# Optimization experiments

Measured on AMD Instinct MI355X. Metric: run time of the kernel, lower is better.

The kernel has to match this reference:

```python
import jax, jax.numpy as jnp
import numpy as np

HOPS = 3  # max_hops; C has HOPS+1 tables

def setup_inputs() -> dict:
    key = jax.random.key(0)
    k1, k2, k3 = jax.random.split(key, 3)
    B, M, S, V, D = 32, 512, 10, 32000, 128
    story = jax.random.randint(k1, (B, M, S), 0, V)
    hidden = jax.random.normal(k2, (B, 1, D), dtype=jnp.float32)
    # hop+1 embedding tables, initialized N(0, 0.1) like the torch module
    C = 0.1 * jax.random.normal(k3, (HOPS + 1, V, D), dtype=jnp.float32)
    return {"story": story, "hidden": hidden, "C": C}

def reference(story, hidden, C):
    # story: [B, M, S] int tokens; hidden: [B, 1, D]; C: [HOPS+1, V, D]
    u = jnp.squeeze(hidden, axis=1)  # [B, D]
    prob_logit = None
    for h in range(HOPS):
        # embedding gather + bag-sum over sentence dim -> [B, M, D]
        embed_A = jnp.take(C[h], story, axis=0).sum(axis=2)
        # dot-product attention logits against current query u
        prob_logit = jnp.einsum('bmd,bd->bm', embed_A, u)  # [B, M]
        prob = jax.nn.softmax(prob_logit, axis=1)
        # second table gather + bag-sum, then softmax-weighted combine
        embed_C = jnp.take(C[h + 1], story, axis=0).sum(axis=2)  # [B, M, D]
        o_k = jnp.einsum('bm,bmd->bd', prob, embed_C)  # [B, D]
        u = u + o_k
    return prob_logit, u
```

## Files before the change

### kernel.cpp

```cpp
#include <hip/hip_runtime.h>

#define BB 32
#define MM 512
#define SS 10
#define VV 32000
#define DD 128
#define HOPS 3
#define BM (BB * MM)
#define NCHUNK 32
#define CHM (MM / NCHUNK)
#define PSTRIDE 132
#define PAIR_UNITS ((size_t)VV * 32)

__device__ __forceinline__ unsigned bfrn(float f) {
    unsigned u = __float_as_uint(f);
    return (u + 0x7FFFu + ((u >> 16) & 1u)) >> 16;
}
__device__ __forceinline__ unsigned pk(float a, float b) { return bfrn(a) | (bfrn(b) << 16); }
__device__ __forceinline__ float bflo(unsigned q) { return __uint_as_float(q << 16); }
__device__ __forceinline__ float bfhi(unsigned q) { return __uint_as_float(q & 0xFFFF0000u); }

__device__ __forceinline__ void cvt_pair_unit(const float* __restrict__ CA,
                                              const float* __restrict__ CB,
                                              unsigned* __restrict__ dst, size_t g) {
    const size_t v = g >> 5, j = g & 31;
    const float4 a = ((const float4*)CA)[v * 32 + j];
    const float4 b = ((const float4*)CB)[v * 32 + j];
    uint4 o;
    o.x = pk(a.x, a.y);
    o.y = pk(b.x, b.y);
    o.z = pk(a.z, a.w);
    o.w = pk(b.z, b.w);
    ((uint4*)dst)[v * 32 + j] = o;
}


__global__ __launch_bounds__(256) void cvt01(const float* __restrict__ Cmat,
                                             unsigned* __restrict__ Cb01) {
    const size_t g = (size_t)blockIdx.x * 256 + threadIdx.x;
    if (g < PAIR_UNITS)
        cvt_pair_unit(Cmat, Cmat + (size_t)VV * DD, Cb01, g);
}

__device__ __forceinline__ void stage_u(const int b, const int c, const int tid,
                                        const float* __restrict__ uprev,
                                        const float* __restrict__ pin,
                                        float* __restrict__ uwrite,
                                        float* __restrict__ su) {
    if (tid < DD) {
        float v = uprev[b * DD + tid];
        if (pin) {
            float num = 0.f, dsum = 0.f;
            for (int cc = 0; cc < NCHUNK; ++cc) {
                const float* p = pin + ((size_t)b * NCHUNK + cc) * PSTRIDE;
                num += p[tid];
                dsum += p[DD];
            }
            v += num / dsum;
            if (c == 0 && uwrite) uwrite[b * DD + tid] = v;
        }
        su[tid] = v;
    }
    __syncthreads();
}

__device__ __forceinline__ void write_partial(const int b, const int c,
                                              const int w, const int lane,
                                              float nx, float ny, float den,
                                              float* __restrict__ pout,
                                              float (*sx)[64], float (*sy)[64],
                                              float* sd) {
    sx[w][lane] = nx; sy[w][lane] = ny;
    if (lane == 0) sd[w] = den;
    __syncthreads();
    if (w == 0) {
        const float ox = sx[0][lane] + sx[1][lane] + sx[2][lane] + sx[3][lane];
        const float oy = sy[0][lane] + sy[1][lane] + sy[2][lane] + sy[3][lane];
        float* prow = pout + ((size_t)b * NCHUNK + c) * PSTRIDE;
        ((float2*)prow)[lane] = make_float2(ox, oy);
        if (lane == 0) prow[DD] = sd[0] + sd[1] + sd[2] + sd[3];
    }
}

__global__ __launch_bounds__(256) void hop0_k(const int* __restrict__ story,
                                              const unsigned* __restrict__ Cb01,
                                              float* __restrict__ E1,
                                              const float* __restrict__ hidden,
                                              float* __restrict__ pout,
                                              const float* __restrict__ Cmat,
                                              unsigned* __restrict__ Cb23) {
    const int b = blockIdx.y, c = blockIdx.x;
    const int tid = threadIdx.x;
    const int w = tid >> 6, lane = tid & 63;
    __shared__ float su[DD];
    __shared__ float sx[4][64], sy[4][64];
    __shared__ float sd[4];

    stage_u(b, c, tid, hidden, nullptr, nullptr, su);
    const float2 uv = ((const float2*)su)[lane];
    const uint2* G = (const uint2*)Cb01;

    float nx = 0.f, ny = 0.f, den = 0.f;
#pragma unroll
    for (int k = 0; k < CHM / 4; ++k) {
        const int m = c * CHM + k * 4 + w;
        const int bm = b * MM + m;
        int tok[SS];
        const int* st = story + (size_t)bm * SS;
#pragma unroll
        for (int s = 0; s < SS; ++s) tok[s] = st[s];

        float ex = 0.f, ey = 0.f, rx = 0.f, ry = 0.f;
#pragma unroll
        for (int s = 0; s < SS; ++s) {
            const uint2 q = G[(size_t)tok[s] * 64 + lane];
            ex += bflo(q.x); ey += bfhi(q.x);
            rx += bflo(q.y); ry += bfhi(q.y);
        }
        float l = ex * uv.x + ey * uv.y;
#pragma unroll
        for (int off = 32; off; off >>= 1) l += __shfl_xor(l, off, 64);
        const float e = expf(l);

        ((float2*)(E1 + (size_t)bm * DD))[lane] = make_float2(rx, ry);
        nx += e * rx; ny += e * ry; den += e;
    }
    write_partial(b, c, w, lane, nx, ny, den, pout, sx, sy, sd);

    const size_t t0 = (((size_t)blockIdx.y * gridDim.x + blockIdx.x) * 256 + tid) * 4;
#pragma unroll
    for (int i = 0; i < 4; ++i) {
        const size_t g = t0 + i;
        if (g < PAIR_UNITS)
            cvt_pair_unit(Cmat + (size_t)2 * VV * DD, Cmat + (size_t)3 * VV * DD,
                          Cb23, g);
    }
}

__global__ __launch_bounds__(256) void hop1_k(const int* __restrict__ story,
                                              const unsigned* __restrict__ Cb23,
                                              const float* __restrict__ E1,
                                              float* __restrict__ E2,
                                              float* __restrict__ E3,
                                              const float* __restrict__ hidden,
                                              const float* __restrict__ pin,
                                              float* __restrict__ u1,
                                              float* __restrict__ pout) {
    const int b = blockIdx.y, c = blockIdx.x;
    const int tid = threadIdx.x;
    const int w = tid >> 6, lane = tid & 63;
    __shared__ float su[DD];
    __shared__ float sx[4][64], sy[4][64];
    __shared__ float sd[4];

    stage_u(b, c, tid, hidden, pin, u1, su);
    const float2 uv = ((const float2*)su)[lane];
    const uint2* G = (const uint2*)Cb23;

    float nx = 0.f, ny = 0.f, den = 0.f;
#pragma unroll
    for (int k = 0; k < CHM / 4; ++k) {
        const int m = c * CHM + k * 4 + w;
        const int bm = b * MM + m;
        int tok[SS];
        const int* st = story + (size_t)bm * SS;
#pragma unroll
        for (int s = 0; s < SS; ++s) tok[s] = st[s];

        const float2 ev = ((const float2*)(E1 + (size_t)bm * DD))[lane];
        float l = ev.x * uv.x + ev.y * uv.y;
#pragma unroll
        for (int off = 32; off; off >>= 1) l += __shfl_xor(l, off, 64);
        const float e = expf(l);

        float r2x = 0.f, r2y = 0.f, r3x = 0.f, r3y = 0.f;
#pragma unroll
        for (int s = 0; s < SS; ++s) {
            const uint2 q = G[(size_t)tok[s] * 64 + lane];
            r2x += bflo(q.x); r2y += bfhi(q.x);
            r3x += bflo(q.y); r3y += bfhi(q.y);
        }
        ((float2*)(E2 + (size_t)bm * DD))[lane] = make_float2(r2x, r2y);
        ((float2*)(E3 + (size_t)bm * DD))[lane] = make_float2(r3x, r3y);
        nx += e * r2x; ny += e * r2y; den += e;
    }
    write_partial(b, c, w, lane, nx, ny, den, pout, sx, sy, sd);
}

__global__ __launch_bounds__(256) void hop2_k(const float* __restrict__ E2,
                                              const float* __restrict__ E3,
                                              const float* __restrict__ u1,
                                              const float* __restrict__ pin,
                                              float* __restrict__ u2,
                                              float* __restrict__ logit,
                                              float* __restrict__ pout) {
    const int b = blockIdx.y, c = blockIdx.x;
    const int tid = threadIdx.x;
    const int w = tid >> 6, lane = tid & 63;
    __shared__ float su[DD];
    __shared__ float sx[4][64], sy[4][64];
    __shared__ float sd[4];

    stage_u(b, c, tid, u1, pin, u2, su);
    const float2 uv = ((const float2*)su)[lane];

    float nx = 0.f, ny = 0.f, den = 0.f;
#pragma unroll
    for (int k = 0; k < CHM / 4; ++k) {
        const int m = c * CHM + k * 4 + w;
        const int bm = b * MM + m;

        const float2 ev = ((const float2*)(E2 + (size_t)bm * DD))[lane];
        float l = ev.x * uv.x + ev.y * uv.y;
#pragma unroll
        for (int off = 32; off; off >>= 1) l += __shfl_xor(l, off, 64);
        if (lane == 0) logit[bm] = l;
        const float e = expf(l);

        const float2 rv = ((const float2*)(E3 + (size_t)bm * DD))[lane];
        nx += e * rv.x; ny += e * rv.y; den += e;
    }
    write_partial(b, c, w, lane, nx, ny, den, pout, sx, sy, sd);
}

__global__ __launch_bounds__(128) void final_u(const float* __restrict__ pin,
                                               const float* __restrict__ u2,
                                               float* __restrict__ uout) {
    const int b = blockIdx.x, d = threadIdx.x;
    float num = 0.f, den = 0.f;
    for (int cc = 0; cc < NCHUNK; ++cc) {
        const float* p = pin + ((size_t)b * NCHUNK + cc) * PSTRIDE;
        num += p[d];
        den += p[DD];
    }
    uout[b * DD + d] = u2[b * DD + d] + num / den;
}

__global__ __launch_bounds__(256) void init_u(const float* __restrict__ hidden,
                                              float* __restrict__ u) {
    int i = blockIdx.x * 256 + threadIdx.x;
    if (i < BB * DD) u[i] = hidden[i];
}

__global__ __launch_bounds__(256) void logit_kernel(const int* __restrict__ story,
                                                    const float* __restrict__ Ch,
                                                    const float* __restrict__ u,
                                                    float* __restrict__ logit) {
    int wid = (blockIdx.x * 256 + threadIdx.x) >> 6;
    int lane = threadIdx.x & 63;
    if (wid >= BB * MM) return;
    int b = wid >> 9;
    const int* st = story + (size_t)wid * SS;
    int tok[SS];
#pragma unroll
    for (int s = 0; s < SS; ++s) tok[s] = st[s];
    float ax = 0.f, ay = 0.f;
#pragma unroll
    for (int s = 0; s < SS; ++s) {
        const float2 v = ((const float2*)(Ch + (size_t)tok[s] * DD))[lane];
        ax += v.x; ay += v.y;
    }
    const float2 uv = ((const float2*)(u + b * DD))[lane];
    float p = ax * uv.x + ay * uv.y;
#pragma unroll
    for (int off = 32; off; off >>= 1) p += __shfl_down(p, off, 64);
    if (lane == 0) logit[wid] = p;
}

__global__ __launch_bounds__(256) void softmax_kernel(const float* __restrict__ logit,
                                                      float* __restrict__ prob) {
    int b = blockIdx.x;
    int t = threadIdx.x;
    __shared__ float red[8];
    float l0 = logit[b * MM + t];
    float l1 = logit[b * MM + 256 + t];
    float mx = fmaxf(l0, l1);
#pragma unroll
    for (int off = 32; off; off >>= 1) mx = fmaxf(mx, __shfl_xor(mx, off, 64));
    if ((t & 63) == 0) red[t >> 6] = mx;
    __syncthreads();
    mx = fmaxf(fmaxf(red[0], red[1]), fmaxf(red[2], red[3]));
    float e0 = expf(l0 - mx), e1 = expf(l1 - mx);
    float s = e0 + e1;
#pragma unroll
    for (int off = 32; off; off >>= 1) s += __shfl_xor(s, off, 64);
    if ((t & 63) == 0) red[4 + (t >> 6)] = s;
    __syncthreads();
    s = red[4] + red[5] + red[6] + red[7];
    float inv = 1.0f / s;
    prob[b * MM + t] = e0 * inv;
    prob[b * MM + 256 + t] = e1 * inv;
}

__global__ __launch_bounds__(256) void partial_kernel(const int* __restrict__ story,
                                                      const float* __restrict__ Ch1,
                                                      const float* __restrict__ prob,
                                                      float* __restrict__ partial,
                                                      int chunk) {
    int b = blockIdx.y, c = blockIdx.x;
    int w = threadIdx.x >> 6, lane = threadIdx.x & 63;
    int m0 = c * chunk;
    float ax = 0.f, ay = 0.f;
    for (int m = m0 + w; m < m0 + chunk; m += 4) {
        float pw = prob[b * MM + m];
        const int* st = story + (size_t)(b * MM + m) * SS;
        int tok[SS];
#pragma unroll
        for (int s = 0; s < SS; ++s) tok[s] = st[s];
        float sx = 0.f, sy = 0.f;
#pragma unroll
        for (int s = 0; s < SS; ++s) {
            const float2 v = ((const float2*)(Ch1 + (size_t)tok[s] * DD))[lane];
            sx += v.x; sy += v.y;
        }
        ax += pw * sx; ay += pw * sy;
    }
    __shared__ float redx[4][64];
    __shared__ float redy[4][64];
    redx[w][lane] = ax;
    redy[w][lane] = ay;
    __syncthreads();
    if (w == 0) {
        float ox = redx[0][lane] + redx[1][lane] + redx[2][lane] + redx[3][lane];
        float oy = redy[0][lane] + redy[1][lane] + redy[2][lane] + redy[3][lane];
        float2* dst = (float2*)(partial + ((size_t)b * gridDim.x + c) * DD);
        dst[lane] = make_float2(ox, oy);
    }
}

__global__ __launch_bounds__(256) void update_kernel(const float* __restrict__ partial,
                                                     float* __restrict__ u, int NC) {
    int i = blockIdx.x * 256 + threadIdx.x;
    if (i >= BB * DD) return;
    int b = i >> 7, d = i & 127;
    float s = 0.f;
    for (int c = 0; c < NC; ++c) s += partial[((size_t)b * NC + c) * DD + d];
    u[i] += s;
}

extern "C" void kernel_launch(void* const* d_in, const int* in_sizes, int n_in,
                              void* d_out, int out_size, void* d_ws, size_t ws_size,
                              hipStream_t stream) {
    const int*   story  = (const int*)d_in[0];
    const float* hidden = (const float*)d_in[1];
    const float* Cmat   = (const float*)d_in[2];

    float* out   = (float*)d_out;
    float* logit = out;
    float* uout  = out + BB * MM;

    const size_t szCbp = (size_t)VV * 128;
    const size_t szE   = (size_t)BM * DD;
    const size_t szP   = (size_t)BB * NCHUNK * PSTRIDE;
    const size_t need  = (2 * szCbp + 3 * szE + 2 * szP + 2 * BB * DD) * sizeof(float);

    if (ws_size >= need) {
        unsigned* Cb01 = (unsigned*)d_ws;
        unsigned* Cb23 = Cb01 + szCbp;
        float* E1 = (float*)d_ws + 2 * szCbp;
        float* E2 = E1 + szE;
        float* E3 = E2 + szE;
        float* Pa = E3 + szE;
        float* Pb = Pa + szP;
        float* u1 = Pb + szP;
        float* u2 = u1 + BB * DD;

        cvt01<<<(unsigned)((PAIR_UNITS + 255) / 256), 256, 0, stream>>>(Cmat, Cb01);
        hop0_k<<<dim3(NCHUNK, BB), 256, 0, stream>>>(story, Cb01, E1, hidden, Pa,
                                                     Cmat, Cb23);
        hop1_k<<<dim3(NCHUNK, BB), 256, 0, stream>>>(story, Cb23, E1, E2, E3,
                                                     hidden, Pa, u1, Pb);
        hop2_k<<<dim3(NCHUNK, BB), 256, 0, stream>>>(E2, E3, u1, Pb, u2, logit, Pa);
        final_u<<<BB, 128, 0, stream>>>(Pa, u2, uout);
    } else {
        float* prob = (float*)d_ws;
        int NC = 32;
        while (NC > 1 && (size_t)(BB * MM + BB * NC * DD) * 4 > ws_size) NC >>= 1;
        float* partial = prob + BB * MM;
        int chunk = MM / NC;

        init_u<<<(BB * DD + 255) / 256, 256, 0, stream>>>(hidden, uout);
        for (int h = 0; h < HOPS; ++h) {
            const float* Ca = Cmat + (size_t)h * VV * DD;
            const float* Cc = Cmat + (size_t)(h + 1) * VV * DD;
            logit_kernel<<<(BB * MM) / 4, 256, 0, stream>>>(story, Ca, uout, logit);
            softmax_kernel<<<BB, 256, 0, stream>>>(logit, prob);
            partial_kernel<<<dim3(NC, BB), 256, 0, stream>>>(story, Cc, prob, partial, chunk);
            update_kernel<<<(BB * DD + 255) / 256, 256, 0, stream>>>(partial, uout, NC);
        }
    }
}
```

Measured before the change: 65.12 us.

## Drop bf16 table conversion; gather fp32 tables directly and fuse final hop

Removes the bf16 pre-conversion of all four embedding tables, which read and wrote about 65 MB of table data on every call, and gathers rows straight from the fp32 tables in the hop kernels. It also merges the last hop and the final u update into one 1024-thread block per batch, removing a launch and the partial buffer round-trip. The cost is twice the bytes per gathered row. The fused last kernel also runs only 32 blocks, so that stage has less parallelism.

```diff
diff --git a/kernel.cpp b/kernel.cpp
--- a/kernel.cpp
+++ b/kernel.cpp
@@ -10,59 +10,7 @@
 #define NCHUNK 32
 #define CHM (MM / NCHUNK)
 #define PSTRIDE 132
-#define PAIR_UNITS ((size_t)VV * 32)
-
-__device__ __forceinline__ unsigned bfrn(float f) {
-    unsigned u = __float_as_uint(f);
-    return (u + 0x7FFFu + ((u >> 16) & 1u)) >> 16;
-}
-__device__ __forceinline__ unsigned pk(float a, float b) { return bfrn(a) | (bfrn(b) << 16); }
-__device__ __forceinline__ float bflo(unsigned q) { return __uint_as_float(q << 16); }
-__device__ __forceinline__ float bfhi(unsigned q) { return __uint_as_float(q & 0xFFFF0000u); }
-
-__device__ __forceinline__ void cvt_pair_unit(const float* __restrict__ CA,
-                                              const float* __restrict__ CB,
-                                              unsigned* __restrict__ dst, size_t g) {
-    const size_t v = g >> 5, j = g & 31;
-    const float4 a = ((const float4*)CA)[v * 32 + j];
-    const float4 b = ((const float4*)CB)[v * 32 + j];
-    uint4 o;
-    o.x = pk(a.x, a.y);
-    o.y = pk(b.x, b.y);
-    o.z = pk(a.z, a.w);
-    o.w = pk(b.z, b.w);
-    ((uint4*)dst)[v * 32 + j] = o;
-}
-
-
-__global__ __launch_bounds__(256) void cvt01(const float* __restrict__ Cmat,
-                                             unsigned* __restrict__ Cb01) {
-    const size_t g = (size_t)blockIdx.x * 256 + threadIdx.x;
-    if (g < PAIR_UNITS)
-        cvt_pair_unit(Cmat, Cmat + (size_t)VV * DD, Cb01, g);
-}
-
-__device__ __forceinline__ void stage_u(const int b, const int c, const int tid,
-                                        const float* __restrict__ uprev,
-                                        const float* __restrict__ pin,
-                                        float* __restrict__ uwrite,
-                                        float* __restrict__ su) {
-    if (tid < DD) {
-        float v = uprev[b * DD + tid];
-        if (pin) {
-            float num = 0.f, dsum = 0.f;
-            for (int cc = 0; cc < NCHUNK; ++cc) {
-                const float* p = pin + ((size_t)b * NCHUNK + cc) * PSTRIDE;
-                num += p[tid];
-                dsum += p[DD];
-            }
-            v += num / dsum;
-            if (c == 0 && uwrite) uwrite[b * DD + tid] = v;
-        }
-        su[tid] = v;
-    }
-    __syncthreads();
-}
+
 
 __device__ __forceinline__ void write_partial(const int b, const int c,
                                               const int w, const int lane,
@@ -83,12 +31,11 @@
 }
 
 __global__ __launch_bounds__(256) void hop0_k(const int* __restrict__ story,
-                                              const unsigned* __restrict__ Cb01,
+                                              const float* __restrict__ C0,
+                                              const float* __restrict__ C1,
+                                              const float* __restrict__ hidden,
                                               float* __restrict__ E1,
-                                              const float* __restrict__ hidden,
-                                              float* __restrict__ pout,
-                                              const float* __restrict__ Cmat,
-                                              unsigned* __restrict__ Cb23) {
+                                              float* __restrict__ P0) {
     const int b = blockIdx.y, c = blockIdx.x;
     const int tid = threadIdx.x;
     const int w = tid >> 6, lane = tid & 63;
@@ -96,9 +43,9 @@
     __shared__ float sx[4][64], sy[4][64];
     __shared__ float sd[4];
 
-    stage_u(b, c, tid, hidden, nullptr, nullptr, su);
+    if (tid < DD) su[tid] = hidden[b * DD + tid];
+    __syncthreads();
     const float2 uv = ((const float2*)su)[lane];
-    const uint2* G = (const uint2*)Cb01;
 
     float nx = 0.f, ny = 0.f, den = 0.f;
 #pragma unroll
@@ -110,42 +57,39 @@
 #pragma unroll
         for (int s = 0; s < SS; ++s) tok[s] = st[s];
 
-        float ex = 0.f, ey = 0.f, rx = 0.f, ry = 0.f;
-#pragma unroll
-        for (int s = 0; s < SS; ++s) {
-            const uint2 q = G[(size_t)tok[s] * 64 + lane];
-            ex += bflo(q.x); ey += bfhi(q.x);
-            rx += bflo(q.y); ry += bfhi(q.y);
+        float ex = 0.f, ey = 0.f;
+#pragma unroll
+        for (int s = 0; s < SS; ++s) {
+            const float2 v = ((const float2*)(C0 + (size_t)tok[s] * DD))[lane];
+            ex += v.x; ey += v.y;
         }
         float l = ex * uv.x + ey * uv.y;
 #pragma unroll
         for (int off = 32; off; off >>= 1) l += __shfl_xor(l, off, 64);
         const float e = expf(l);
 
+        float rx = 0.f, ry = 0.f;
+#pragma unroll
+        for (int s = 0; s < SS; ++s) {
+            const float2 v = ((const float2*)(C1 + (size_t)tok[s] * DD))[lane];
+            rx += v.x; ry += v.y;
+        }
         ((float2*)(E1 + (size_t)bm * DD))[lane] = make_float2(rx, ry);
         nx += e * rx; ny += e * ry; den += e;
     }
-    write_partial(b, c, w, lane, nx, ny, den, pout, sx, sy, sd);
-
-    const size_t t0 = (((size_t)blockIdx.y * gridDim.x + blockIdx.x) * 256 + tid) * 4;
-#pragma unroll
-    for (int i = 0; i < 4; ++i) {
-        const size_t g = t0 + i;
-        if (g < PAIR_UNITS)
-            cvt_pair_unit(Cmat + (size_t)2 * VV * DD, Cmat + (size_t)3 * VV * DD,
-                          Cb23, g);
-    }
+    write_partial(b, c, w, lane, nx, ny, den, P0, sx, sy, sd);
 }
 
 __global__ __launch_bounds__(256) void hop1_k(const int* __restrict__ story,
-                                              const unsigned* __restrict__ Cb23,
+                                              const float* __restrict__ C2,
+                                              const float* __restrict__ C3,
                                               const float* __restrict__ E1,
+                                              const float* __restrict__ hidden,
+                                              const float* __restrict__ P0,
+                                              float* __restrict__ u1,
                                               float* __restrict__ E2,
                                               float* __restrict__ E3,
-                                              const float* __restrict__ hidden,
-                                              const float* __restrict__ pin,
-                                              float* __restrict__ u1,
-                                              float* __restrict__ pout) {
+                                              float* __restrict__ P1) {
     const int b = blockIdx.y, c = blockIdx.x;
     const int tid = threadIdx.x;
     const int w = tid >> 6, lane = tid & 63;
@@ -153,9 +97,19 @@
     __shared__ float sx[4][64], sy[4][64];
     __shared__ float sd[4];
 
-    stage_u(b, c, tid, hidden, pin, u1, su);
+    if (tid < DD) {
+        float num = 0.f, dsum = 0.f;
+        for (int cc = 0; cc < NCHUNK; ++cc) {
+            const float* p = P0 + ((size_t)b * NCHUNK + cc) * PSTRIDE;
+            num += p[tid];
+            dsum += p[DD];
+        }
+        const float v = hidden[b * DD + tid] + num / dsum;
+        if (c == 0) u1[b * DD + tid] = v;
+        su[tid] = v;
+    }
+    __syncthreads();
     const float2 uv = ((const float2*)su)[lane];
-    const uint2* G = (const uint2*)Cb23;
 
     float nx = 0.f, ny = 0.f, den = 0.f;
 #pragma unroll
@@ -173,67 +127,74 @@
         for (int off = 32; off; off >>= 1) l += __shfl_xor(l, off, 64);
         const float e = expf(l);
 
-        float r2x = 0.f, r2y = 0.f, r3x = 0.f, r3y = 0.f;
-#pragma unroll
-        for (int s = 0; s < SS; ++s) {
-            const uint2 q = G[(size_t)tok[s] * 64 + lane];
-            r2x += bflo(q.x); r2y += bfhi(q.x);
-            r3x += bflo(q.y); r3y += bfhi(q.y);
+        float r2x = 0.f, r2y = 0.f;
+#pragma unroll
+        for (int s = 0; s < SS; ++s) {
+            const float2 v = ((const float2*)(C2 + (size_t)tok[s] * DD))[lane];
+            r2x += v.x; r2y += v.y;
+        }
+        float r3x = 0.f, r3y = 0.f;
+#pragma unroll
+        for (int s = 0; s < SS; ++s) {
+            const float2 v = ((const float2*)(C3 + (size_t)tok[s] * DD))[lane];
+            r3x += v.x; r3y += v.y;
         }
         ((float2*)(E2 + (size_t)bm * DD))[lane] = make_float2(r2x, r2y);
         ((float2*)(E3 + (size_t)bm * DD))[lane] = make_float2(r3x, r3y);
         nx += e * r2x; ny += e * r2y; den += e;
     }
-    write_partial(b, c, w, lane, nx, ny, den, pout, sx, sy, sd);
-}
-
-__global__ __launch_bounds__(256) void hop2_k(const float* __restrict__ E2,
-                                              const float* __restrict__ E3,
-                                              const float* __restrict__ u1,
-                                              const float* __restrict__ pin,
-                                              float* __restrict__ u2,
-                                              float* __restrict__ logit,
-                                              float* __restrict__ pout) {
-    const int b = blockIdx.y, c = blockIdx.x;
+    write_partial(b, c, w, lane, nx, ny, den, P1, sx, sy, sd);
+}
+
+__global__ __launch_bounds__(1024) void hop2_final(const float* __restrict__ E2,
+                                                   const float* __restrict__ E3,
+                                                   const float* __restrict__ u1,
+                                                   const float* __restrict__ P1,
+                                                   float* __restrict__ logit,
+                                                   float* __restrict__ uout) {
+    const int b = blockIdx.x;
     const int tid = threadIdx.x;
     const int w = tid >> 6, lane = tid & 63;
     __shared__ float su[DD];
-    __shared__ float sx[4][64], sy[4][64];
-    __shared__ float sd[4];
-
-    stage_u(b, c, tid, u1, pin, u2, su);
+    __shared__ float sx[16][64], sy[16][64];
+    __shared__ float sd[16];
+
+    if (tid < DD) {
+        float num = 0.f, dsum = 0.f;
+        for (int cc = 0; cc < NCHUNK; ++cc) {
+            const float* p = P1 + ((size_t)b * NCHUNK + cc) * PSTRIDE;
+            num += p[tid];
+            dsum += p[DD];
+        }
+        su[tid] = u1[b * DD + tid] + num / dsum;
+    }
+    __syncthreads();
     const float2 uv = ((const float2*)su)[lane];
 
     float nx = 0.f, ny = 0.f, den = 0.f;
-#pragma unroll
-    for (int k = 0; k < CHM / 4; ++k) {
-        const int m = c * CHM + k * 4 + w;
+#pragma unroll 4
+    for (int m = w * 32; m < w * 32 + 32; ++m) {
         const int bm = b * MM + m;
-
         const float2 ev = ((const float2*)(E2 + (size_t)bm * DD))[lane];
         float l = ev.x * uv.x + ev.y * uv.y;
 #pragma unroll
         for (int off = 32; off; off >>= 1) l += __shfl_xor(l, off, 64);
         if (lane == 0) logit[bm] = l;
         const float e = expf(l);
-
         const float2 rv = ((const float2*)(E3 + (size_t)bm * DD))[lane];
         nx += e * rv.x; ny += e * rv.y; den += e;
     }
-    write_partial(b, c, w, lane, nx, ny, den, pout, sx, sy, sd);
-}
-
-__global__ __launch_bounds__(128) void final_u(const float* __restrict__ pin,
-                                               const float* __restrict__ u2,
-                                               float* __restrict__ uout) {
-    const int b = blockIdx.x, d = threadIdx.x;
-    float num = 0.f, den = 0.f;
-    for (int cc = 0; cc < NCHUNK; ++cc) {
-        const float* p = pin + ((size_t)b * NCHUNK + cc) * PSTRIDE;
-        num += p[d];
-        den += p[DD];
-    }
-    uout[b * DD + d] = u2[b * DD + d] + num / den;
+
+    sx[w][lane] = nx; sy[w][lane] = ny;
+    if (lane == 0) sd[w] = den;
+    __syncthreads();
+    if (w == 0) {
+        float ox = 0.f, oy = 0.f, od = 0.f;
+#pragma unroll
+        for (int i = 0; i < 16; ++i) { ox += sx[i][lane]; oy += sy[i][lane]; od += sd[i]; }
+        const float2 u2 = ((const float2*)su)[lane];
+        ((float2*)(uout + b * DD))[lane] = make_float2(u2.x + ox / od, u2.y + oy / od);
+    }
 }
 
 __global__ __launch_bounds__(256) void init_u(const float* __restrict__ hidden,
@@ -349,29 +310,27 @@
     float* logit = out;
     float* uout  = out + BB * MM;
 
-    const size_t szCbp = (size_t)VV * 128;
-    const size_t szE   = (size_t)BM * DD;
-    const size_t szP   = (size_t)BB * NCHUNK * PSTRIDE;
-    const size_t need  = (2 * szCbp + 3 * szE + 2 * szP + 2 * BB * DD) * sizeof(float);
+    const size_t szE  = (size_t)BM * DD;
+    const size_t szP  = (size_t)BB * NCHUNK * PSTRIDE;
+    const size_t need = (3 * szE + 2 * szP + BB * DD) * sizeof(float);
 
     if (ws_size >= need) {
-        unsigned* Cb01 = (unsigned*)d_ws;
-        unsigned* Cb23 = Cb01 + szCbp;
-        float* E1 = (float*)d_ws + 2 * szCbp;
+        float* E1 = (float*)d_ws;
         float* E2 = E1 + szE;
         float* E3 = E2 + szE;
-        float* Pa = E3 + szE;
-        float* Pb = Pa + szP;
-        float* u1 = Pb + szP;
-        float* u2 = u1 + BB * DD;
-
-        cvt01<<<(unsigned)((PAIR_UNITS + 255) / 256), 256, 0, stream>>>(Cmat, Cb01);
-        hop0_k<<<dim3(NCHUNK, BB), 256, 0, stream>>>(story, Cb01, E1, hidden, Pa,
-                                                     Cmat, Cb23);
-        hop1_k<<<dim3(NCHUNK, BB), 256, 0, stream>>>(story, Cb23, E1, E2, E3,
-                                                     hidden, Pa, u1, Pb);
-        hop2_k<<<dim3(NCHUNK, BB), 256, 0, stream>>>(E2, E3, u1, Pb, u2, logit, Pa);
-        final_u<<<BB, 128, 0, stream>>>(Pa, u2, uout);
+        float* P0 = E3 + szE;
+        float* P1 = P0 + szP;
+        float* u1 = P1 + szP;
+
+        const float* C0 = Cmat;
+        const float* C1 = Cmat + (size_t)1 * VV * DD;
+        const float* C2 = Cmat + (size_t)2 * VV * DD;
+        const float* C3 = Cmat + (size_t)3 * VV * DD;
+
+        hop0_k<<<dim3(NCHUNK, BB), 256, 0, stream>>>(story, C0, C1, hidden, E1, P0);
+        hop1_k<<<dim3(NCHUNK, BB), 256, 0, stream>>>(story, C2, C3, E1, hidden,
+                                                     P0, u1, E2, E3, P1);
+        hop2_final<<<BB, 1024, 0, stream>>>(E2, E3, u1, P1, logit, uout);
     } else {
         float* prob = (float*)d_ws;
         int NC = 32;
```

New measurement: 77.44 us. +18.9%, slower.
